# Performance work log

Measured on AMD Instinct MI355X. Metric: run time of the kernel, lower is better.

Reference implementation:

```python
import jax, jax.numpy as jnp
import numpy as np
from jax import lax

ANCHOR_NUM = 5
OUTPUT_NUM = 4  # 'reg' branch


def setup_inputs() -> dict:
    key = jax.random.key(0)
    k1, k2 = jax.random.split(key)
    detection = jax.random.normal(k1, (64, 20, 20, 256), dtype=jnp.float32)
    templates = jax.random.normal(k2, (64, 4, 4, 256 * ANCHOR_NUM * OUTPUT_NUM), dtype=jnp.float32)
    return {"detection": detection, "templates": templates}


def reference(detection, templates):
    # detection: [B, Hd, Wd, C]; templates: [B, Hk, Wk, C * O]
    # Original TF code fakes per-example-kernel conv via one big depthwise_conv2d
    # followed by reduce_sum over channel groups. Mathematically:
    #   out[b, y, x, o] = sum_{i,j,c} detection[b, y+i, x+j, c] * tmpl[b, i, j, c, o]
    # i.e. a per-example VALID cross-correlation. We express it as a vmapped conv.
    B, Hd, Wd, C = detection.shape
    _, Hk, Wk, CO = templates.shape
    O = CO // C  # anchor_num * output_num = 20
    tmpl = templates.reshape(B, Hk, Wk, C, O)

    def corr_one(det, ker):
        # det: [Hd, Wd, C], ker: [Hk, Wk, C, O] -> [Ho, Wo, O]
        out = lax.conv_general_dilated(
            det[None],  # [1, Hd, Wd, C]
            ker,        # HWIO
            window_strides=(1, 1),
            padding="VALID",
            dimension_numbers=("NHWC", "HWIO", "NHWC"),
        )
        return out[0]

    out = jax.vmap(corr_one)(detection, tmpl)  # [B, Ho, Wo, O]
    return out
```

## Files before the change

kernel.cpp:

```cpp
#include <hip/hip_runtime.h>
#include <hip/hip_bf16.h>


typedef __bf16 bf16x8 __attribute__((ext_vector_type(8)));
typedef float f32x4 __attribute__((ext_vector_type(4)));

#define NB 64
#define C_TOT 256
#define CQ 32
#define NQ 8
#define NPOS 400
#define NP 289
#define NO 20
#define PTILE (NP * NO)
#define DET_LDS_BYTES (NPOS * CQ * 2)
#define TMP_LDS_BYTES (16 * 32 * CQ * 2)

__device__ __forceinline__ unsigned short bfbits(float f) {
  __bf16 h = (__bf16)f;
  return __builtin_bit_cast(unsigned short, h);
}

__global__ __launch_bounds__(256)
void reduce_kernel(const float4* __restrict__ ws, float4* __restrict__ out, int n4) {
  int i = blockIdx.x * 256 + threadIdx.x;
  if (i >= n4) return;
  float4 s = ws[i];
  #pragma unroll
  for (int q = 1; q < NQ; ++q) {
    float4 v = ws[q * n4 + i];
    s.x += v.x; s.y += v.y; s.z += v.z; s.w += v.w;
  }
  out[i] = s;
}

__global__ __launch_bounds__(512, 4)
void siamese_kernel(const float* __restrict__ det,
                    const float* __restrict__ tmp,
                    float* __restrict__ ws) {
  __shared__ alignas(16) char lds[DET_LDS_BYTES + TMP_LDS_BYTES];
  char* detB = lds;
  char* tmpB = lds + DET_LDS_BYTES;

  const int tid = threadIdx.x;
  const int b   = blockIdx.x >> 3;
  const int q   = blockIdx.x & 7;
  const int c0  = q * CQ;

  {
    const float* __restrict__ dsrc = det + (size_t)b * (NPOS * C_TOT);
    for (int it = tid; it < NPOS * CQ / 4; it += 512) {
      int pos = it >> 3;
      int cg  = it & 7;
      const float4 v = *(const float4*)(dsrc + pos * C_TOT + c0 + cg * 4);
      unsigned long long pk =
          (unsigned long long)bfbits(v.x) |
          ((unsigned long long)bfbits(v.y) << 16) |
          ((unsigned long long)bfbits(v.z) << 32) |
          ((unsigned long long)bfbits(v.w) << 48);
      int byte = pos * 64 + (((cg >> 1) ^ ((pos >> 1) & 3)) << 4) + (cg & 1) * 8;
      *(unsigned long long*)(detB + byte) = pk;
    }
  }

  {
    for (int z = tid; z < 16 * 12 * 4; z += 512) {
      int rr = z >> 2;
      int ij = rr / 12;
      int o  = 20 + (rr % 12);
      int byte = (ij * 32 + o) * 64 + (z & 3) * 16;
      *(uint4*)(tmpB + byte) = make_uint4(0u, 0u, 0u, 0u);
    }
  }

  {
    const float* __restrict__ tsrc = tmp + (size_t)b * (16 * C_TOT * NO);
    for (int it = tid; it < 16 * CQ * 5; it += 512) {
      int og = it % 5;
      int c  = (it / 5) & 31;
      int ij = it / 160;
      const float4 v = *(const float4*)(tsrc + ij * (C_TOT * NO) + (c0 + c) * NO + og * 4);
      unsigned short s4[4] = { bfbits(v.x), bfbits(v.y), bfbits(v.z), bfbits(v.w) };
      int gbase = ((c & 7) * 2) + ((c >> 3) << 4);
      #pragma unroll
      for (int k = 0; k < 4; ++k) {
        int o    = og * 4 + k;
        int byte = (ij * 32 + o) * 64 + (gbase ^ (((o >> 1) & 3) << 4));
        *(unsigned short*)(tmpB + byte) = s4[k];
      }
    }
  }

  __syncthreads();

  const int w    = tid >> 6;
  const int lane = tid & 63;
  const int lo   = lane & 15;
  const int hi   = lane >> 4;
  const int nm   = (w < 3) ? 3 : 2;

  int posb[3];
  #pragma unroll
  for (int mi = 0; mi < 3; ++mi) {
    int m = w + mi * 8;
    int p = m * 16 + lo;
    if (p > NP - 1) p = NP - 1;
    posb[mi] = (p / 17) * 20 + (p % 17);
  }

  f32x4 acc[3][2] = {};

  const int o0   = lo;
  const int o1   = 16 + lo;
  const int bad0 = o0 * 64 + ((hi ^ ((o0 >> 1) & 3)) << 4);
  const int bad1 = o1 * 64 + ((hi ^ ((o1 >> 1) & 3)) << 4);

  for (int ij = 0; ij < 16; ++ij) {
    const int i  = ij >> 2, j = ij & 3;
    const int sh = i * 20 + j;

    bf16x8 bf0 = *(const bf16x8*)(tmpB + bad0 + ij * (32 * 64));
    bf16x8 bf1 = *(const bf16x8*)(tmpB + bad1 + ij * (32 * 64));

    bf16x8 a[3];
    #pragma unroll
    for (int mi = 0; mi < 3; ++mi) {
      if (mi < nm) {
        int pos  = posb[mi] + sh;
        int byte = pos * 64 + ((hi ^ ((pos >> 1) & 3)) << 4);
        a[mi] = *(const bf16x8*)(detB + byte);
      }
    }
    #pragma unroll
    for (int mi = 0; mi < 3; ++mi) {
      if (mi < nm) {
        acc[mi][0] = __builtin_amdgcn_mfma_f32_16x16x32_bf16(a[mi], bf0, acc[mi][0], 0, 0, 0);
        acc[mi][1] = __builtin_amdgcn_mfma_f32_16x16x32_bf16(a[mi], bf1, acc[mi][1], 0, 0, 0);
      }
    }
  }

  float* __restrict__ pws = ws + ((size_t)q * NB + b) * PTILE;
  #pragma unroll
  for (int mi = 0; mi < 3; ++mi) {
    if (mi < nm) {
      int m = w + mi * 8;
      #pragma unroll
      for (int n = 0; n < 2; ++n) {
        int o = n * 16 + lo;
        if (o < NO) {
          #pragma unroll
          for (int v = 0; v < 4; ++v) {
            int p = m * 16 + hi * 4 + v;
            if (p < NP) pws[p * NO + o] = acc[mi][n][v];
          }
        }
      }
    }
  }
}

extern "C" void kernel_launch(void* const* d_in, const int* in_sizes, int n_in,
                              void* d_out, int out_size, void* d_ws, size_t ws_size,
                              hipStream_t stream) {
  (void)in_sizes; (void)n_in; (void)ws_size;
  const float* det = (const float*)d_in[0];
  const float* tmp = (const float*)d_in[1];
  float* out = (float*)d_out;
  float* ws  = (float*)d_ws;

  siamese_kernel<<<dim3(NB * NQ), dim3(512), 0, stream>>>(det, tmp, ws);
  int n4 = out_size / 4;
  reduce_kernel<<<dim3((n4 + 255) / 256), dim3(256), 0, stream>>>(
      (const float4*)ws, (float4*)out, n4);
}
```

Measured before the change: 21.91 us.

## Halve block size, pad template LDS to 24 outputs, batch global loads

Cuts the workgroup from 512 to 256 threads, so each wave now owns 5 (or 4) M-tiles instead of 3 (or 2), and launch bounds change to 3 blocks per CU. The template LDS buffer is padded to 24 output rows instead of 32, with out-of-range output lanes clamped to the last row, and the explicit zero-fill pass is dropped. Detection loads are issued in unrolled batches of six float4s before their LDS writes, and each thread now loads 20 contiguous template floats. The aim is more memory-level parallelism and a smaller LDS footprint. The cost is more accumulator registers per thread and garbage values in the unused padded output columns, which are never stored.

```diff
diff --git a/kernel.cpp b/kernel.cpp
--- a/kernel.cpp
+++ b/kernel.cpp
@@ -12,9 +12,10 @@
 #define NPOS 400
 #define NP 289
 #define NO 20
+#define OPAD 24
 #define PTILE (NP * NO)
 #define DET_LDS_BYTES (NPOS * CQ * 2)
-#define TMP_LDS_BYTES (16 * 32 * CQ * 2)
+#define TMP_LDS_BYTES (16 * OPAD * CQ * 2)
 
 __device__ __forceinline__ unsigned short bfbits(float f) {
   __bf16 h = (__bf16)f;
@@ -34,7 +35,18 @@
   out[i] = s;
 }
 
-__global__ __launch_bounds__(512, 4)
+__device__ __forceinline__ void det_write(char* detB, int it, float4 v) {
+  int pos = it >> 3, cg = it & 7;
+  unsigned long long pk =
+      (unsigned long long)bfbits(v.x) |
+      ((unsigned long long)bfbits(v.y) << 16) |
+      ((unsigned long long)bfbits(v.z) << 32) |
+      ((unsigned long long)bfbits(v.w) << 48);
+  int byte = pos * 64 + (((cg >> 1) ^ ((pos >> 1) & 3)) << 4) + (cg & 1) * 8;
+  *(unsigned long long*)(detB + byte) = pk;
+}
+
+__global__ __launch_bounds__(256, 3)
 void siamese_kernel(const float* __restrict__ det,
                     const float* __restrict__ tmp,
                     float* __restrict__ ws) {
@@ -47,46 +59,54 @@
   const int q   = blockIdx.x & 7;
   const int c0  = q * CQ;
 
+  const float* __restrict__ dsrc = det + (size_t)b * (NPOS * C_TOT) + c0;
+  const float* __restrict__ tsrc = tmp + (size_t)b * (16 * C_TOT * NO);
+
   {
-    const float* __restrict__ dsrc = det + (size_t)b * (NPOS * C_TOT);
-    for (int it = tid; it < NPOS * CQ / 4; it += 512) {
-      int pos = it >> 3;
-      int cg  = it & 7;
-      const float4 v = *(const float4*)(dsrc + pos * C_TOT + c0 + cg * 4);
-      unsigned long long pk =
-          (unsigned long long)bfbits(v.x) |
-          ((unsigned long long)bfbits(v.y) << 16) |
-          ((unsigned long long)bfbits(v.z) << 32) |
-          ((unsigned long long)bfbits(v.w) << 48);
-      int byte = pos * 64 + (((cg >> 1) ^ ((pos >> 1) & 3)) << 4) + (cg & 1) * 8;
-      *(unsigned long long*)(detB + byte) = pk;
+    float4 v[6];
+    #pragma unroll
+    for (int k = 0; k < 6; ++k) {
+      int it = tid + k * 256;
+      v[k] = *(const float4*)(dsrc + (it >> 3) * C_TOT + (it & 7) * 4);
     }
+    #pragma unroll
+    for (int k = 0; k < 6; ++k) det_write(detB, tid + k * 256, v[k]);
+    #pragma unroll
+    for (int k = 0; k < 6; ++k) {
+      int it = tid + (k + 6) * 256;
+      v[k] = *(const float4*)(dsrc + (it >> 3) * C_TOT + (it & 7) * 4);
+    }
+    float4 vt;
+    if (tid < 128) {
+      int it = 3072 + tid;
+      vt = *(const float4*)(dsrc + (it >> 3) * C_TOT + (it & 7) * 4);
+    }
+    #pragma unroll
+    for (int k = 0; k < 6; ++k) det_write(detB, tid + (k + 6) * 256, v[k]);
+    if (tid < 128) det_write(detB, 3072 + tid, vt);
   }
 
   {
-    for (int z = tid; z < 16 * 12 * 4; z += 512) {
-      int rr = z >> 2;
-      int ij = rr / 12;
-      int o  = 20 + (rr % 12);
-      int byte = (ij * 32 + o) * 64 + (z & 3) * 16;
-      *(uint4*)(tmpB + byte) = make_uint4(0u, 0u, 0u, 0u);
-    }
-  }
-
-  {
-    const float* __restrict__ tsrc = tmp + (size_t)b * (16 * C_TOT * NO);
-    for (int it = tid; it < 16 * CQ * 5; it += 512) {
-      int og = it % 5;
-      int c  = (it / 5) & 31;
-      int ij = it / 160;
-      const float4 v = *(const float4*)(tsrc + ij * (C_TOT * NO) + (c0 + c) * NO + og * 4);
-      unsigned short s4[4] = { bfbits(v.x), bfbits(v.y), bfbits(v.z), bfbits(v.w) };
-      int gbase = ((c & 7) * 2) + ((c >> 3) << 4);
+    #pragma unroll
+    for (int pp = 0; pp < 2; ++pp) {
+      int pr = tid + pp * 256;
+      int ij = pr >> 5, c = pr & 31;
+      const float* s = tsrc + ij * (C_TOT * NO) + (c0 + c) * NO;
+      float4 u[5];
       #pragma unroll
-      for (int k = 0; k < 4; ++k) {
-        int o    = og * 4 + k;
-        int byte = (ij * 32 + o) * 64 + (gbase ^ (((o >> 1) & 3) << 4));
-        *(unsigned short*)(tmpB + byte) = s4[k];
+      for (int k = 0; k < 5; ++k) u[k] = *(const float4*)(s + k * 4);
+      unsigned short sv[20];
+      #pragma unroll
+      for (int k = 0; k < 5; ++k) {
+        sv[k*4+0] = bfbits(u[k].x); sv[k*4+1] = bfbits(u[k].y);
+        sv[k*4+2] = bfbits(u[k].z); sv[k*4+3] = bfbits(u[k].w);
+      }
+      char* base = tmpB + ij * (OPAD * 64) + (c & 7) * 2;
+      int g = (c >> 3) << 4;
+      #pragma unroll
+      for (int o = 0; o < NO; ++o) {
+        int byte = o * 64 + (g ^ (((o >> 1) & 3) << 4));
+        *(unsigned short*)(base + byte) = sv[o];
       }
     }
   }
@@ -97,54 +117,47 @@
   const int lane = tid & 63;
   const int lo   = lane & 15;
   const int hi   = lane >> 4;
-  const int nm   = (w < 3) ? 3 : 2;
+  const int nm   = (w < 3) ? 5 : 4;
 
-  int posb[3];
+  int posb[5];
   #pragma unroll
-  for (int mi = 0; mi < 3; ++mi) {
-    int m = w + mi * 8;
+  for (int mi = 0; mi < 5; ++mi) {
+    int m = w + mi * 4;
     int p = m * 16 + lo;
     if (p > NP - 1) p = NP - 1;
     posb[mi] = (p / 17) * 20 + (p % 17);
   }
 
-  f32x4 acc[3][2] = {};
+  f32x4 acc[5][2] = {};
 
-  const int o0   = lo;
-  const int o1   = 16 + lo;
-  const int bad0 = o0 * 64 + ((hi ^ ((o0 >> 1) & 3)) << 4);
-  const int bad1 = o1 * 64 + ((hi ^ ((o1 >> 1) & 3)) << 4);
+  const int o0r  = lo;
+  const int o1r  = (16 + lo < OPAD) ? (16 + lo) : (OPAD - 1);
+  const int bad0 = o0r * 64 + ((hi ^ ((o0r >> 1) & 3)) << 4);
+  const int bad1 = o1r * 64 + ((hi ^ ((o1r >> 1) & 3)) << 4);
 
   for (int ij = 0; ij < 16; ++ij) {
-    const int i  = ij >> 2, j = ij & 3;
-    const int sh = i * 20 + j;
+    const int sh = (ij >> 2) * 20 + (ij & 3);
 
-    bf16x8 bf0 = *(const bf16x8*)(tmpB + bad0 + ij * (32 * 64));
-    bf16x8 bf1 = *(const bf16x8*)(tmpB + bad1 + ij * (32 * 64));
+    bf16x8 bf0 = *(const bf16x8*)(tmpB + bad0 + ij * (OPAD * 64));
+    bf16x8 bf1 = *(const bf16x8*)(tmpB + bad1 + ij * (OPAD * 64));
 
-    bf16x8 a[3];
     #pragma unroll
-    for (int mi = 0; mi < 3; ++mi) {
+    for (int mi = 0; mi < 5; ++mi) {
       if (mi < nm) {
         int pos  = posb[mi] + sh;
         int byte = pos * 64 + ((hi ^ ((pos >> 1) & 3)) << 4);
-        a[mi] = *(const bf16x8*)(detB + byte);
-      }
-    }
-    #pragma unroll
-    for (int mi = 0; mi < 3; ++mi) {
-      if (mi < nm) {
-        acc[mi][0] = __builtin_amdgcn_mfma_f32_16x16x32_bf16(a[mi], bf0, acc[mi][0], 0, 0, 0);
-        acc[mi][1] = __builtin_amdgcn_mfma_f32_16x16x32_bf16(a[mi], bf1, acc[mi][1], 0, 0, 0);
+        bf16x8 a = *(const bf16x8*)(detB + byte);
+        acc[mi][0] = __builtin_amdgcn_mfma_f32_16x16x32_bf16(a, bf0, acc[mi][0], 0, 0, 0);
+        acc[mi][1] = __builtin_amdgcn_mfma_f32_16x16x32_bf16(a, bf1, acc[mi][1], 0, 0, 0);
       }
     }
   }
 
   float* __restrict__ pws = ws + ((size_t)q * NB + b) * PTILE;
   #pragma unroll
-  for (int mi = 0; mi < 3; ++mi) {
+  for (int mi = 0; mi < 5; ++mi) {
     if (mi < nm) {
-      int m = w + mi * 8;
+      int m = w + mi * 4;
       #pragma unroll
       for (int n = 0; n < 2; ++n) {
         int o = n * 16 + lo;
@@ -169,7 +182,7 @@
   float* out = (float*)d_out;
   float* ws  = (float*)d_ws;
 
-  siamese_kernel<<<dim3(NB * NQ), dim3(512), 0, stream>>>(det, tmp, ws);
+  siamese_kernel<<<dim3(NB * NQ), dim3(256), 0, stream>>>(det, tmp, ws);
   int n4 = out_size / 4;
   reduce_kernel<<<dim3((n4 + 255) / 256), dim3(256), 0, stream>>>(
       (const float4*)ws, (float4*)out, n4);
```

Measured after the change: 23.09 us. 1.05x slower.
